# Kernel optimization log

Hardware: AMD Instinct MI355X
Metric: run time of the kernel (lower is better)

Reference implementation:

```python
import jax, jax.numpy as jnp
import numpy as np

B, T, D, H = 4, 4096, 1024, 16
HD = D // H  # head_dim = 64


def setup_inputs() -> dict:
    key = jax.random.key(0)
    k1, k2, k3 = jax.random.split(key, 3)
    x = jax.random.normal(k1, (B, T, D), dtype=jnp.float32)
    # torch Linear weight is (out,in); we store transposed (in,out) for x @ W
    Wqkv = jax.random.normal(k2, (D, 3 * D), dtype=jnp.float32) * 0.02
    Wout = jax.random.normal(k3, (D, D), dtype=jnp.float32) * 0.02
    return {"x": x, "Wqkv": Wqkv, "Wout": Wout}


def reference(x, Wqkv, Wout):
    # Faithful to original: qkv reshaped to (B,T,3,H,hd) WITHOUT moving heads to
    # a batch dim, so attention mixes the H heads of each token (scores: B,T,H,H).
    qkv = (x @ Wqkv).reshape(B, T, 3, H, HD)
    q, k, v = qkv[:, :, 0], qkv[:, :, 1], qkv[:, :, 2]  # each (B,T,H,HD)
    scores = jnp.einsum('btid,btjd->btij', q, k) / jnp.sqrt(jnp.float32(HD))
    attn = jax.nn.softmax(scores, axis=-1)  # softmax over heads j
    out = jnp.einsum('btij,btjd->btid', attn, v).reshape(B, T, D)
    return out @ Wout
```

## Files before the change

### kernel.cpp

```cpp
#include <hip/hip_runtime.h>
#include <hip/hip_bf16.h>
#include <cstdint>
#include <cstddef>


typedef __bf16 bf16x8 __attribute__((ext_vector_type(8)));
typedef __bf16 bf16x4 __attribute__((ext_vector_type(4)));
typedef float  f32x4  __attribute__((ext_vector_type(4)));

#define AS1 __attribute__((address_space(1)))
#define AS3 __attribute__((address_space(3)))

__device__ __forceinline__ void async_copy16(const void* g, void* l) {
    __builtin_amdgcn_global_load_lds((const AS1 void*)g, (AS3 void*)l, 16, 0, 0);
}

__device__ __forceinline__ int invp_qkv(int col) {
    int g = col >> 10;
    if (g == 2) { int q = col & 1023; return 2048 + ((q & 63) << 4) + (q >> 6); }
    int h = (col >> 6) & 15, d = col & 63;
    return (g << 10) + ((d & 32) << 4) + (((d >> 3) & 3) << 7) + (h << 3) + (d & 7);
}

__device__ __forceinline__ int invp_ao(int k) {
    return (((k >> 8) & 3) << 8) + ((k & 15) << 4) + (((k >> 4) & 3) << 2) + ((k >> 6) & 3);
}

__global__ __launch_bounds__(256) void cvt_bf16_kernel(const float4* __restrict__ in,
                                                       bf16x4* __restrict__ out, int n4) {
    int i = blockIdx.x * 256 + threadIdx.x;
    if (i >= n4) return;
    float4 v = in[i];
    bf16x4 o = { (__bf16)v.x, (__bf16)v.y, (__bf16)v.z, (__bf16)v.w };
    out[i] = o;
}

__global__ __launch_bounds__(256) void transpose_qkv_kernel(const float* __restrict__ in,
                                                            __bf16* __restrict__ out) {
    __shared__ float tile[32][33];
    const int C = 3072;
    int c0 = blockIdx.x * 32, r0 = blockIdx.y * 32;
    int tx = threadIdx.x, ty = threadIdx.y;
    #pragma unroll
    for (int i = 0; i < 32; i += 8)
        tile[ty + i][tx] = in[(size_t)(r0 + ty + i) * C + c0 + tx];
    __syncthreads();
    #pragma unroll
    for (int i = 0; i < 32; i += 8) {
        int prow = invp_qkv(c0 + ty + i);
        out[(size_t)prow * 1024 + r0 + tx] = (__bf16)tile[tx][ty + i];
    }
}

__global__ __launch_bounds__(256) void transpose_wout_kernel(const float* __restrict__ in,
                                                             __bf16* __restrict__ out) {
    __shared__ float tile[32][33];
    const int C = 1024;
    int c0 = blockIdx.x * 32, r0 = blockIdx.y * 32;
    int tx = threadIdx.x, ty = threadIdx.y;
    #pragma unroll
    for (int i = 0; i < 32; i += 8)
        tile[ty + i][tx] = in[(size_t)(r0 + ty + i) * C + c0 + tx];
    __syncthreads();
    int pk = invp_ao(r0 + tx);
    #pragma unroll
    for (int i = 0; i < 32; i += 8)
        out[(size_t)(c0 + ty + i) * 1024 + pk] = (__bf16)tile[tx][ty + i];
}

template<int OUT_BF16>
__global__ __launch_bounds__(512, 2) void gemm_bt(const __bf16* __restrict__ A,
                                                  const __bf16* __restrict__ Bt,
                                                  void* __restrict__ Cv,
                                                  int N, int K) {
    __shared__ __attribute__((aligned(16))) __bf16 As[3 * 256 * 32];
    __shared__ __attribute__((aligned(16))) __bf16 Bs[3 * 256 * 32];

    const int lin = blockIdx.x;
    const int xcd = lin & 7;
    const int rr  = lin >> 3;
    const int by  = xcd * 8 + (rr & 7);
    const int bx  = rr >> 3;

    const int tid  = threadIdx.x;
    const int wave = tid >> 6;
    const int lane = tid & 63;
    const int quad = lane >> 4;
    const int q16  = lane & 15;
    const int wr   = wave >> 2, wc = wave & 3;
    const int row0 = by * 256;
    const int col0 = bx * 256;

    const __bf16* Ag = A  + (size_t)row0 * K;
    const __bf16* Bg = Bt + (size_t)col0 * K;

    const int srow = tid >> 2;
    const int sk   = ((tid & 3) ^ ((srow >> 1) & 3)) << 3;
    const __bf16* aSrc = Ag + (size_t)srow * K + sk;
    const __bf16* bSrc = Bg + (size_t)srow * K + sk;
    char* aDst = (char*)As + tid * 16;
    char* bDst = (char*)Bs + tid * 16;

    const int pxo  = (quad ^ ((q16 >> 1) & 3)) << 4;
    const int aoff = wr * 8192 + q16 * 64 + pxo;
    const int boff = wc * 4096 + q16 * 64 + pxo;

    f32x4 acc[8][4] = {};

    const int NT = K >> 5;

#define STAGE(t) do { \
        const size_t so_ = (size_t)(t) * 32; \
        const int   sl_  = (t) % 3; \
        async_copy16(aSrc + so_,                   aDst + sl_ * 16384); \
        async_copy16(aSrc + (size_t)128 * K + so_, aDst + sl_ * 16384 + 8192); \
        async_copy16(bSrc + so_,                   bDst + sl_ * 16384); \
        async_copy16(bSrc + (size_t)128 * K + so_, bDst + sl_ * 16384 + 8192); \
    } while (0)

    STAGE(0);
    STAGE(1);
    asm volatile("s_waitcnt vmcnt(4)" ::: "memory");
    __builtin_amdgcn_s_barrier();
    __builtin_amdgcn_sched_barrier(0);

    #pragma unroll 1
    for (int t = 0; t < NT; ++t) {
        if (t + 2 < NT) STAGE(t + 2);
        const int slot = t % 3;
        const char* Ab = (const char*)As + slot * 16384;
        const char* Bb = (const char*)Bs + slot * 16384;
        bf16x8 af[8], bf[4];
        #pragma unroll
        for (int mi = 0; mi < 8; ++mi)
            af[mi] = *(const bf16x8*)(Ab + aoff + mi * 1024);
        #pragma unroll
        for (int ni = 0; ni < 4; ++ni)
            bf[ni] = *(const bf16x8*)(Bb + boff + ni * 1024);
        __builtin_amdgcn_s_setprio(1);
        #pragma unroll
        for (int mi = 0; mi < 8; ++mi)
            #pragma unroll
            for (int ni = 0; ni < 4; ++ni)
                acc[mi][ni] = __builtin_amdgcn_mfma_f32_16x16x32_bf16(af[mi], bf[ni], acc[mi][ni], 0, 0, 0);
        __builtin_amdgcn_s_setprio(0);
        __builtin_amdgcn_sched_barrier(0);
        if (t < NT - 2) asm volatile("s_waitcnt vmcnt(4)" ::: "memory");
        else            asm volatile("s_waitcnt vmcnt(0)" ::: "memory");
        __builtin_amdgcn_s_barrier();
        __builtin_amdgcn_sched_barrier(0);
    }
#undef STAGE

    #pragma unroll
    for (int mi = 0; mi < 8; ++mi) {
        #pragma unroll
        for (int ni = 0; ni < 4; ++ni) {
            const int col = col0 + wc * 64 + ni * 16 + q16;
            #pragma unroll
            for (int r = 0; r < 4; ++r) {
                const int row = row0 + wr * 128 + mi * 16 + quad * 4 + r;
                if (OUT_BF16)
                    ((__bf16*)Cv)[(size_t)row * N + col] = (__bf16)acc[mi][ni][r];
                else
                    ((float*)Cv)[(size_t)row * N + col] = acc[mi][ni][r];
            }
        }
    }
}

__global__ __launch_bounds__(256) void attn_mfma_kernel(const __bf16* __restrict__ qkv,
                                                        __bf16* __restrict__ ao) {
    const int tok  = blockIdx.x * 4 + (threadIdx.x >> 6);
    const int lane = threadIdx.x & 63;
    const int quad = lane >> 4;
    const int q16  = lane & 15;

    const __bf16* base = qkv + (size_t)tok * 3072;

    const bf16x8 qf0 = *(const bf16x8*)(base + lane * 8);
    const bf16x8 qf1 = *(const bf16x8*)(base + 512 + lane * 8);
    const bf16x8 kf0 = *(const bf16x8*)(base + 1024 + lane * 8);
    const bf16x8 kf1 = *(const bf16x8*)(base + 1536 + lane * 8);

    f32x4 st = {0.f, 0.f, 0.f, 0.f};
    st = __builtin_amdgcn_mfma_f32_16x16x32_bf16(kf0, qf0, st, 0, 0, 0);
    st = __builtin_amdgcn_mfma_f32_16x16x32_bf16(kf1, qf1, st, 0, 0, 0);

    float s0 = st[0] * 0.125f, s1 = st[1] * 0.125f, s2 = st[2] * 0.125f, s3 = st[3] * 0.125f;
    float m = fmaxf(fmaxf(s0, s1), fmaxf(s2, s3));
    m = fmaxf(m, __shfl_xor(m, 16));
    m = fmaxf(m, __shfl_xor(m, 32));
    float e0 = __expf(s0 - m), e1 = __expf(s1 - m), e2 = __expf(s2 - m), e3 = __expf(s3 - m);
    float sum = e0 + e1 + e2 + e3;
    sum += __shfl_xor(sum, 16);
    sum += __shfl_xor(sum, 32);
    const float inv = 1.f / sum;

    union { __bf16 h[2]; int i; } u01, u23;
    u01.h[0] = (__bf16)(e0 * inv); u01.h[1] = (__bf16)(e1 * inv);
    u23.h[0] = (__bf16)(e2 * inv); u23.h[1] = (__bf16)(e3 * inv);

    const int src0 = quad * 32 + q16;
    const int src1 = src0 + 16;
    union { int i[4]; bf16x8 v; } af;
    af.i[0] = __shfl(u01.i, src0);
    af.i[1] = __shfl(u23.i, src0);
    af.i[2] = __shfl(u01.i, src1);
    af.i[3] = __shfl(u23.i, src1);
    if (quad >= 2) { af.i[0] = 0; af.i[1] = 0; af.i[2] = 0; af.i[3] = 0; }

    const __bf16* vb = base + 2048;
    f32x4 accs[4];
    #pragma unroll
    for (int c = 0; c < 4; ++c) {
        bf16x8 bfv = {};
        if (quad < 2)
            bfv = *(const bf16x8*)(vb + (c * 16 + q16) * 16 + quad * 8);
        f32x4 z = {0.f, 0.f, 0.f, 0.f};
        accs[c] = __builtin_amdgcn_mfma_f32_16x16x32_bf16(af.v, bfv, z, 0, 0, 0);
    }

    union { __bf16 h[16]; bf16x8 v[2]; } o;
    #pragma unroll
    for (int c = 0; c < 4; ++c)
        #pragma unroll
        for (int r = 0; r < 4; ++r)
            o.h[c * 4 + r] = (__bf16)accs[c][r];
    __bf16* outp = ao + (size_t)tok * 1024 + lane * 16;
    *(bf16x8*)outp = o.v[0];
    *(bf16x8*)(outp + 8) = o.v[1];
}

extern "C" void kernel_launch(void* const* d_in, const int* in_sizes, int n_in,
                              void* d_out, int out_size, void* d_ws, size_t ws_size,
                              hipStream_t stream) {
    const float* x    = (const float*)d_in[0];
    const float* Wqkv = (const float*)d_in[1];
    const float* Wout = (const float*)d_in[2];
    float* out = (float*)d_out;

    char* ws = (char*)d_ws;
    __bf16* xb    = (__bf16*)(ws);
    __bf16* wqkvT = (__bf16*)(ws + 33554432);
    __bf16* woutT = (__bf16*)(ws + 33554432 + 6291456);
    __bf16* qkv   = (__bf16*)(ws + 33554432 + 6291456 + 2097152);
    __bf16* ao    = (__bf16*)(ws + 33554432 + 6291456 + 2097152 + 100663296);

    cvt_bf16_kernel<<<16384, 256, 0, stream>>>((const float4*)x, (bf16x4*)xb, 4194304);
    transpose_qkv_kernel<<<dim3(96, 32), dim3(32, 8), 0, stream>>>(Wqkv, wqkvT);
    transpose_wout_kernel<<<dim3(32, 32), dim3(32, 8), 0, stream>>>(Wout, woutT);
    gemm_bt<1><<<768, 512, 0, stream>>>(xb, wqkvT, (void*)qkv, 3072, 1024);
    attn_mfma_kernel<<<4096, 256, 0, stream>>>(qkv, ao);
    gemm_bt<0><<<256, 512, 0, stream>>>(ao, woutT, (void*)out, 1024, 1024);
}
```

Before: 329.2 us.

## Restructure GEMM main loop into single-buffer BK=64 quadrant-staged pipeline

Replaces the triple-buffered BK=32 LDS ring with a single 256x64 buffer per operand. Each K-step is split into four MFMA quadrants, and the next tile's async loads for a region are issued as soon as the current step's reads of that region finish, with barriers between phases. The aim is to halve the number of outer iterations, give each wave more MFMA work per synchronisation, and reuse LDS in place. The cost is more barriers per iteration and a fragile vmcnt/lgkmcnt ordering that could expose load latency or race on LDS.

```diff
diff --git a/kernel.cpp b/kernel.cpp
--- a/kernel.cpp
+++ b/kernel.cpp
@@ -73,8 +73,8 @@
                                                   const __bf16* __restrict__ Bt,
                                                   void* __restrict__ Cv,
                                                   int N, int K) {
-    __shared__ __attribute__((aligned(16))) __bf16 As[3 * 256 * 32];
-    __shared__ __attribute__((aligned(16))) __bf16 Bs[3 * 256 * 32];
+    __shared__ __attribute__((aligned(16))) __bf16 As[256 * 64];
+    __shared__ __attribute__((aligned(16))) __bf16 Bs[256 * 64];
 
     const int lin = blockIdx.x;
     const int xcd = lin & 7;
@@ -94,63 +94,133 @@
     const __bf16* Ag = A  + (size_t)row0 * K;
     const __bf16* Bg = Bt + (size_t)col0 * K;
 
-    const int srow = tid >> 2;
-    const int sk   = ((tid & 3) ^ ((srow >> 1) & 3)) << 3;
-    const __bf16* aSrc = Ag + (size_t)srow * K + sk;
-    const __bf16* bSrc = Bg + (size_t)srow * K + sk;
-    char* aDst = (char*)As + tid * 16;
-    char* bDst = (char*)Bs + tid * 16;
-
-    const int pxo  = (quad ^ ((q16 >> 1) & 3)) << 4;
-    const int aoff = wr * 8192 + q16 * 64 + pxo;
-    const int boff = wc * 4096 + q16 * 64 + pxo;
+    const int rowIdx = tid >> 3;
+    const int slotq  = tid & 7;
+    const int skel   = ((slotq ^ (rowIdx & 7)) << 3);
+    const int brg    = rowIdx + (rowIdx & 32);
+    const __bf16* aSrc = Ag + (size_t)rowIdx * K + skel;
+    const __bf16* bSrc = Bg + (size_t)brg * K + skel;
+    char* aDst = (char*)As + rowIdx * 128 + slotq * 16;
+    char* bDst = (char*)Bs + brg * 128 + slotq * 16;
+
+    const int px0   = ((quad ^ (q16 & 7)) << 4);
+    const int px1   = px0 ^ 64;
+    const int aBase = (wr * 128 + q16) * 128;
+    const int bBase = (wc * 64 + q16) * 128;
+    const char* AsB = (const char*)As;
+    const char* BsB = (const char*)Bs;
 
     f32x4 acc[8][4] = {};
-
-    const int NT = K >> 5;
-
-#define STAGE(t) do { \
-        const size_t so_ = (size_t)(t) * 32; \
-        const int   sl_  = (t) % 3; \
-        async_copy16(aSrc + so_,                   aDst + sl_ * 16384); \
-        async_copy16(aSrc + (size_t)128 * K + so_, aDst + sl_ * 16384 + 8192); \
-        async_copy16(bSrc + so_,                   bDst + sl_ * 16384); \
-        async_copy16(bSrc + (size_t)128 * K + so_, bDst + sl_ * 16384 + 8192); \
+    bf16x8 af[4][2], bf[4][2];
+
+    const int NT = K >> 6;
+
+#define STAGE_A(t, u) do { \
+        const size_t ko_ = (size_t)(t) * 64; \
+        const int b0_ = (u) ? 64 : 0, b1_ = (u) ? 192 : 128; \
+        async_copy16(aSrc + (size_t)b0_ * K + ko_, aDst + b0_ * 128); \
+        async_copy16(aSrc + (size_t)b1_ * K + ko_, aDst + b1_ * 128); \
     } while (0)
-
-    STAGE(0);
-    STAGE(1);
-    asm volatile("s_waitcnt vmcnt(4)" ::: "memory");
+#define STAGE_B(t, u) do { \
+        const size_t ko_ = (size_t)(t) * 64; \
+        const int s0_ = (u) ? 32 : 0, s1_ = (u) ? 160 : 128; \
+        async_copy16(bSrc + (size_t)s0_ * K + ko_, bDst + s0_ * 128); \
+        async_copy16(bSrc + (size_t)s1_ * K + ko_, bDst + s1_ * 128); \
+    } while (0)
+#define SB0() __builtin_amdgcn_sched_barrier(0)
+#define MFMA_Q(a, b) do { \
+        _Pragma("unroll") \
+        for (int kk = 0; kk < 2; ++kk) \
+            _Pragma("unroll") \
+            for (int mi = 0; mi < 4; ++mi) \
+                _Pragma("unroll") \
+                for (int ni = (b)*2; ni < (b)*2 + 2; ++ni) \
+                    acc[(a)*4 + mi][ni] = __builtin_amdgcn_mfma_f32_16x16x32_bf16( \
+                        af[mi][kk], bf[ni][kk], acc[(a)*4 + mi][ni], 0, 0, 0); \
+    } while (0)
+
+    STAGE_A(0, 0); STAGE_B(0, 0); STAGE_B(0, 1); STAGE_A(0, 1);
+    asm volatile("s_waitcnt vmcnt(0)" ::: "memory");
     __builtin_amdgcn_s_barrier();
-    __builtin_amdgcn_sched_barrier(0);
+    SB0();
 
     #pragma unroll 1
     for (int t = 0; t < NT; ++t) {
-        if (t + 2 < NT) STAGE(t + 2);
-        const int slot = t % 3;
-        const char* Ab = (const char*)As + slot * 16384;
-        const char* Bb = (const char*)Bs + slot * 16384;
-        bf16x8 af[8], bf[4];
-        #pragma unroll
-        for (int mi = 0; mi < 8; ++mi)
-            af[mi] = *(const bf16x8*)(Ab + aoff + mi * 1024);
-        #pragma unroll
-        for (int ni = 0; ni < 4; ++ni)
-            bf[ni] = *(const bf16x8*)(Bb + boff + ni * 1024);
+        const size_t pf = (t + 1 < NT);
+
+        #pragma unroll
+        for (int mi = 0; mi < 4; ++mi) {
+            af[mi][0] = *(const bf16x8*)(AsB + aBase + mi * 2048 + px0);
+            af[mi][1] = *(const bf16x8*)(AsB + aBase + mi * 2048 + px1);
+        }
+        #pragma unroll
+        for (int ni = 0; ni < 2; ++ni) {
+            bf[ni][0] = *(const bf16x8*)(BsB + bBase + ni * 2048 + px0);
+            bf[ni][1] = *(const bf16x8*)(BsB + bBase + ni * 2048 + px1);
+        }
+        SB0();
+        __builtin_amdgcn_s_barrier();
+        asm volatile("s_waitcnt lgkmcnt(0)" ::: "memory");
+        SB0();
         __builtin_amdgcn_s_setprio(1);
-        #pragma unroll
-        for (int mi = 0; mi < 8; ++mi)
-            #pragma unroll
-            for (int ni = 0; ni < 4; ++ni)
-                acc[mi][ni] = __builtin_amdgcn_mfma_f32_16x16x32_bf16(af[mi], bf[ni], acc[mi][ni], 0, 0, 0);
+        MFMA_Q(0, 0);
         __builtin_amdgcn_s_setprio(0);
-        __builtin_amdgcn_sched_barrier(0);
-        if (t < NT - 2) asm volatile("s_waitcnt vmcnt(4)" ::: "memory");
-        else            asm volatile("s_waitcnt vmcnt(0)" ::: "memory");
-        __builtin_amdgcn_s_barrier();
-        __builtin_amdgcn_sched_barrier(0);
+        SB0();
+        asm volatile("s_waitcnt vmcnt(2)" ::: "memory");
+        __builtin_amdgcn_s_barrier();
+        SB0();
+
+        #pragma unroll
+        for (int ni = 2; ni < 4; ++ni) {
+            bf[ni][0] = *(const bf16x8*)(BsB + bBase + ni * 2048 + px0);
+            bf[ni][1] = *(const bf16x8*)(BsB + bBase + ni * 2048 + px1);
+        }
+        if (pf) STAGE_A(t + 1, 0);
+        SB0();
+        __builtin_amdgcn_s_barrier();
+        asm volatile("s_waitcnt lgkmcnt(0)" ::: "memory");
+        SB0();
+        __builtin_amdgcn_s_setprio(1);
+        MFMA_Q(0, 1);
+        __builtin_amdgcn_s_setprio(0);
+        SB0();
+        asm volatile("s_waitcnt vmcnt(2)" ::: "memory");
+        __builtin_amdgcn_s_barrier();
+        SB0();
+
+        #pragma unroll
+        for (int mi = 0; mi < 4; ++mi) {
+            af[mi][0] = *(const bf16x8*)(AsB + aBase + 8192 + mi * 2048 + px0);
+            af[mi][1] = *(const bf16x8*)(AsB + aBase + 8192 + mi * 2048 + px1);
+        }
+        if (pf) { STAGE_B(t + 1, 0); STAGE_B(t + 1, 1); }
+        SB0();
+        __builtin_amdgcn_s_barrier();
+        asm volatile("s_waitcnt lgkmcnt(0)" ::: "memory");
+        SB0();
+        __builtin_amdgcn_s_setprio(1);
+        MFMA_Q(1, 0);
+        __builtin_amdgcn_s_setprio(0);
+        SB0();
+        __builtin_amdgcn_s_barrier();
+        SB0();
+
+        if (pf) STAGE_A(t + 1, 1);
+        SB0();
+        __builtin_amdgcn_s_barrier();
+        SB0();
+        __builtin_amdgcn_s_setprio(1);
+        MFMA_Q(1, 1);
+        __builtin_amdgcn_s_setprio(0);
+        SB0();
+        asm volatile("s_waitcnt vmcnt(4)" ::: "memory");
+        __builtin_amdgcn_s_barrier();
+        SB0();
     }
-#undef STAGE
+#undef MFMA_Q
+#undef SB0
+#undef STAGE_B
+#undef STAGE_A
 
     #pragma unroll
     for (int mi = 0; mi < 8; ++mi) {
```

Result: faster. 296.3 us (-10.0%).
